# Performance work log

Hardware: AMD Instinct MI355X
Metric: run time of the kernel (lower is better)

The kernel has to match this reference:

```python
import jax, jax.numpy as jnp
import numpy as np

B, N, DIM = 2, 2048, 1024
H, DH = 16, 64
INNER = H * DH
SCALE = DH ** -0.5


def rotate_half(x):
    x1, x2 = jnp.split(x, 2, axis=-1)
    return jnp.concatenate((-x2, x1), axis=-1)


def apply_rotary(pos, t):
    # pos: [n, dh] broadcast against t: [b, h, n, dh]
    return t * jnp.cos(pos) + rotate_half(t) * jnp.sin(pos)


def setup_inputs() -> dict:
    key = jax.random.key(0)
    ks = jax.random.split(key, 5)
    x = jax.random.normal(ks[0], (B, N, DIM), dtype=jnp.float32)
    rotary_emb = jax.random.normal(ks[1], (N, DH), dtype=jnp.float32)
    w_qkv = jax.random.normal(ks[2], (3 * INNER, DIM), dtype=jnp.float32) * (DIM ** -0.5)
    w_out = jax.random.normal(ks[3], (DIM, INNER), dtype=jnp.float32) * (INNER ** -0.5)
    b_out = jax.random.normal(ks[4], (DIM,), dtype=jnp.float32) * 0.01
    return {"x": x, "rotary_emb": rotary_emb, "w_qkv": w_qkv, "w_out": w_out, "b_out": b_out}


def reference(x, rotary_emb, w_qkv, w_out, b_out):
    b, n, _ = x.shape
    qkv = jnp.einsum('bnd,ed->bne', x, w_qkv)  # [b, n, 3*inner]
    q, k, v = jnp.split(qkv, 3, axis=-1)
    # [b, n, inner] -> [b, h, n, dh]
    reshape = lambda t: t.reshape(b, n, H, DH).transpose(0, 2, 1, 3)
    q, k, v = reshape(q), reshape(k), reshape(v)
    q = apply_rotary(rotary_emb, q)
    k = apply_rotary(rotary_emb, k)
    dots = jnp.einsum('bhid,bhjd->bhij', q, k) * SCALE
    attn = jax.nn.softmax(dots, axis=-1)
    out = jnp.einsum('bhij,bhjd->bhid', attn, v)
    out = out.transpose(0, 2, 1, 3).reshape(b, n, INNER)
    return jnp.einsum('bne,de->bnd', out, w_out) + b_out
```

## Files before the change

kernel.cpp:

```cpp
#include <hip/hip_runtime.h>
#include <math.h>

typedef unsigned short ushort_t;
typedef __attribute__((ext_vector_type(8))) short short8v;
typedef __attribute__((ext_vector_type(4))) float float4v;

#define BB 2
#define NN 2048
#define HH 16
#define DHH 64
#define DIMM 1024
#define QKV3 3072
#define INNERR 1024
#define QSCALE 0.1803368801111244f

__device__ __forceinline__ ushort_t f2bf(float f) {
    unsigned u = __float_as_uint(f);
    u += 0x7fffu + ((u >> 16) & 1u);
    return (ushort_t)(u >> 16);
}
__device__ __forceinline__ float bf2f(unsigned h) {
    return __uint_as_float(h << 16);
}
__device__ __forceinline__ unsigned pk_bf16(float a, float b) {
#if __has_builtin(__builtin_amdgcn_cvt_pk_bf16_f32)
    typedef __attribute__((ext_vector_type(2))) __bf16 bf16x2;
    bf16x2 r = __builtin_amdgcn_cvt_pk_bf16_f32(a, b);
    return __builtin_bit_cast(unsigned, r);
#else
    return (unsigned)f2bf(a) | ((unsigned)f2bf(b) << 16);
#endif
}
__device__ __forceinline__ float fast_exp2(float x) {
#if __has_builtin(__builtin_amdgcn_exp2f)
    return __builtin_amdgcn_exp2f(x);
#else
    return exp2f(x);
#endif
}
__device__ __forceinline__ void gl2lds16(const void* g, void* l) {
    __builtin_amdgcn_global_load_lds(
        (const __attribute__((address_space(1))) unsigned int*)g,
        (__attribute__((address_space(3))) unsigned int*)l, 16, 0, 0);
}

__global__ __launch_bounds__(256) void conv_fused(const float* __restrict__ x,
                                                  const float* __restrict__ wqkv,
                                                  const float* __restrict__ wout,
                                                  ushort_t* __restrict__ xo,
                                                  ushort_t* __restrict__ wqkvo,
                                                  ushort_t* __restrict__ wouto) {
    int blk = blockIdx.x;
    const float* in; ushort_t* out; int i;
    if (blk < 4096)      { in = x;    out = xo;    i = blk * 256 + threadIdx.x; }
    else if (blk < 7168) { in = wqkv; out = wqkvo; i = (blk - 4096) * 256 + threadIdx.x; }
    else                 { in = wout; out = wouto; i = (blk - 7168) * 256 + threadIdx.x; }
    float4 v = ((const float4*)in)[i];
    ushort4 o;
    o.x = f2bf(v.x); o.y = f2bf(v.y); o.z = f2bf(v.z); o.w = f2bf(v.w);
    ((ushort4*)out)[i] = o;
}

template <int NOUT, bool BF16OUT, bool BIAS, bool ROT>
__global__ __launch_bounds__(256, 3) void gemm128(const ushort_t* __restrict__ A,
                                                  const ushort_t* __restrict__ Bm,
                                                  const float* __restrict__ bias,
                                                  const float* __restrict__ rot,
                                                  ushort_t* __restrict__ Vt,
                                                  void* __restrict__ Cout, int K) {
    constexpr int NCH = 4;
    __shared__ ushort_t As[2][128 * 32];
    __shared__ ushort_t Bs[2][128 * 32];
    const int t = threadIdx.x;
    const int lane = t & 63;
    const int w = t >> 6;
    const int wr = w >> 1;
    const int wc = w & 1;
    const int quad = lane >> 4;
    const int l15 = lane & 15;
    const int m0 = blockIdx.y * 128;
    const int n0 = blockIdx.x * 128;

    float4v acc[4][4];
#pragma unroll
    for (int i = 0; i < 4; ++i)
#pragma unroll
        for (int j = 0; j < 4; ++j) acc[i][j] = (float4v)0.0f;

    int srow[NCH], slc[NCH], sdst[NCH];
    bool sisA[NCH];
#pragma unroll
    for (int u = 0; u < NCH; ++u) {
        int c = u * 256 + t;
        if (c < 512) {
            int row = c >> 2;
            sisA[u] = true; srow[u] = row; slc[u] = (c & 3) ^ ((row >> 1) & 3); sdst[u] = c * 8;
        } else {
            int cb = c - 512;
            int row = cb >> 2;
            sisA[u] = false; srow[u] = row; slc[u] = (cb & 3) ^ ((row >> 1) & 3); sdst[u] = cb * 8;
        }
    }
#pragma unroll
    for (int u = 0; u < NCH; ++u) {
        if (sisA[u]) gl2lds16(&A[(size_t)(m0 + srow[u]) * K + slc[u] * 8], &As[0][sdst[u]]);
        else         gl2lds16(&Bm[(size_t)(n0 + srow[u]) * K + slc[u] * 8], &Bs[0][sdst[u]]);
    }
    const int NIT = K >> 5;
    for (int it = 0; it < NIT; ++it) {
        const int cur = it & 1;
        if (it + 1 < NIT) {
            const int nxt = cur ^ 1;
            const int kc = (it + 1) << 5;
#pragma unroll
            for (int u = 0; u < NCH; ++u) {
                if (sisA[u]) gl2lds16(&A[(size_t)(m0 + srow[u]) * K + kc + slc[u] * 8], &As[nxt][sdst[u]]);
                else         gl2lds16(&Bm[(size_t)(n0 + srow[u]) * K + kc + slc[u] * 8], &Bs[nxt][sdst[u]]);
            }
            asm volatile("s_waitcnt vmcnt(4)\n\ts_barrier" ::: "memory");
        } else {
            asm volatile("s_waitcnt vmcnt(0)\n\ts_barrier" ::: "memory");
        }
        short8v a[4], b[4];
#pragma unroll
        for (int i = 0; i < 4; ++i) {
            int row = wr * 64 + i * 16 + l15;
            int pc = quad ^ ((row >> 1) & 3);
            a[i] = *(const short8v*)&As[cur][row * 32 + pc * 8];
        }
#pragma unroll
        for (int j = 0; j < 4; ++j) {
            int row = wc * 64 + j * 16 + l15;
            int pc = quad ^ ((row >> 1) & 3);
            b[j] = *(const short8v*)&Bs[cur][row * 32 + pc * 8];
        }
#pragma unroll
        for (int i = 0; i < 4; ++i)
#pragma unroll
            for (int j = 0; j < 4; ++j)
                acc[i][j] = __builtin_amdgcn_mfma_f32_16x16x32_bf16(a[i], b[j], acc[i][j], 0, 0, 0);
        asm volatile("s_barrier" ::: "memory");
    }
    const int region = ROT ? (n0 >> 10) : 0;
    if (ROT && region == 2) {
#pragma unroll
        for (int i = 0; i < 4; ++i) {
            int grow = m0 + wr * 64 + i * 16 + quad * 4;
            int bb = grow >> 11, nn_ = grow & (NN - 1);
            int tk = nn_ & 63;
            int tp = (tk & 32) | ((tk & 12) << 1) | ((tk & 16) >> 2);
            int nstore = (nn_ & ~63) | tp;
#pragma unroll
            for (int j = 0; j < 4; ++j) {
                int vcol = n0 + wc * 64 + j * 16 + l15 - 2048;
                int hh = vcol >> 6, dh = vcol & 63;
                uint2 st;
                st.x = pk_bf16(acc[i][j][0], acc[i][j][1]);
                st.y = pk_bf16(acc[i][j][2], acc[i][j][3]);
                *(uint2*)&Vt[((size_t)(bb * HH + hh) * DHH + dh) * NN + nstore] = st;
            }
        }
        return;
    }
    if (ROT) {
        float scale = (region == 0) ? QSCALE : 1.0f;
#pragma unroll
        for (int i = 0; i < 4; ++i) {
#pragma unroll
            for (int r = 0; r < 4; ++r) {
                int n = (m0 + wr * 64 + i * 16 + quad * 4 + r) & (NN - 1);
#pragma unroll
                for (int jl = 0; jl < 2; ++jl) {
                    int dh = jl * 16 + l15;
                    float plo = rot[n * DHH + dh];
                    float phi = rot[n * DHH + dh + 32];
                    float lo = acc[i][jl][r], hi = acc[i][jl + 2][r];
                    acc[i][jl][r]     = (lo * __cosf(plo) - hi * __sinf(plo)) * scale;
                    acc[i][jl + 2][r] = (hi * __cosf(phi) + lo * __sinf(phi)) * scale;
                }
            }
        }
    }
#pragma unroll
    for (int i = 0; i < 4; ++i) {
        int grow = m0 + wr * 64 + i * 16 + quad * 4;
#pragma unroll
        for (int j = 0; j < 4; ++j) {
            int gcol = n0 + wc * 64 + j * 16 + l15;
            float bv = BIAS ? bias[gcol] : 0.0f;
#pragma unroll
            for (int r = 0; r < 4; ++r) {
                float v = acc[i][j][r] + bv;
                if (BF16OUT)
                    ((ushort_t*)Cout)[(size_t)(grow + r) * NOUT + gcol] = f2bf(v);
                else
                    ((float*)Cout)[(size_t)(grow + r) * NOUT + gcol] = v;
            }
        }
    }
}

template <int NOUT, bool BF16OUT, bool BIAS, bool ROT>
__global__ __launch_bounds__(256, 6) void gemm_bf16(const ushort_t* __restrict__ A,
                                                    const ushort_t* __restrict__ Bm,
                                                    const float* __restrict__ bias,
                                                    const float* __restrict__ rot,
                                                    ushort_t* __restrict__ Vt,
                                                    void* __restrict__ Cout, int K) {
    constexpr int NCH = 3;
    __shared__ ushort_t As[2][128 * 32];
    __shared__ ushort_t Bs[2][64 * 32];
    const int t = threadIdx.x;
    const int lane = t & 63;
    const int w = t >> 6;
    const int quad = lane >> 4;
    const int l15 = lane & 15;
    const int m0 = blockIdx.y * 128;
    const int n0 = blockIdx.x * 64;
    const int wm = w * 32;

    float4v acc[2][4];
#pragma unroll
    for (int i = 0; i < 2; ++i)
#pragma unroll
        for (int j = 0; j < 4; ++j) acc[i][j] = (float4v)0.0f;

    int srow[NCH], slc[NCH], sdst[NCH];
    bool sisA[NCH];
#pragma unroll
    for (int u = 0; u < NCH; ++u) {
        int c = u * 256 + t;
        if (c < 512) {
            int row = c >> 2;
            sisA[u] = true; srow[u] = row; slc[u] = (c & 3) ^ ((row >> 1) & 3); sdst[u] = c * 8;
        } else {
            int cb = c - 512;
            int row = cb >> 2;
            sisA[u] = false; srow[u] = row; slc[u] = (cb & 3) ^ ((row >> 1) & 3); sdst[u] = cb * 8;
        }
    }
#pragma unroll
    for (int u = 0; u < NCH; ++u) {
        if (sisA[u]) gl2lds16(&A[(size_t)(m0 + srow[u]) * K + slc[u] * 8], &As[0][sdst[u]]);
        else         gl2lds16(&Bm[(size_t)(n0 + srow[u]) * K + slc[u] * 8], &Bs[0][sdst[u]]);
    }
    const int NIT = K >> 5;
    for (int it = 0; it < NIT; ++it) {
        const int cur = it & 1;
        if (it + 1 < NIT) {
            const int nxt = cur ^ 1;
            const int kc = (it + 1) << 5;
#pragma unroll
            for (int u = 0; u < NCH; ++u) {
                if (sisA[u]) gl2lds16(&A[(size_t)(m0 + srow[u]) * K + kc + slc[u] * 8], &As[nxt][sdst[u]]);
                else         gl2lds16(&Bm[(size_t)(n0 + srow[u]) * K + kc + slc[u] * 8], &Bs[nxt][sdst[u]]);
            }
            asm volatile("s_waitcnt vmcnt(3)\n\ts_barrier" ::: "memory");
        } else {
            asm volatile("s_waitcnt vmcnt(0)\n\ts_barrier" ::: "memory");
        }
        short8v a[2], b[4];
#pragma unroll
        for (int i = 0; i < 2; ++i) {
            int row = wm + i * 16 + l15;
            int pc = quad ^ ((row >> 1) & 3);
            a[i] = *(const short8v*)&As[cur][row * 32 + pc * 8];
        }
#pragma unroll
        for (int j = 0; j < 4; ++j) {
            int row = j * 16 + l15;
            int pc = quad ^ ((row >> 1) & 3);
            b[j] = *(const short8v*)&Bs[cur][row * 32 + pc * 8];
        }
#pragma unroll
        for (int i = 0; i < 2; ++i)
#pragma unroll
            for (int j = 0; j < 4; ++j)
                acc[i][j] = __builtin_amdgcn_mfma_f32_16x16x32_bf16(a[i], b[j], acc[i][j], 0, 0, 0);
        asm volatile("s_barrier" ::: "memory");
    }
#pragma unroll
    for (int i = 0; i < 2; ++i) {
        int grow = m0 + wm + i * 16 + quad * 4;
#pragma unroll
        for (int j = 0; j < 4; ++j) {
            int gcol = n0 + j * 16 + l15;
            float bv = BIAS ? bias[gcol] : 0.0f;
#pragma unroll
            for (int r = 0; r < 4; ++r) {
                float v = acc[i][j][r] + bv;
                if (BF16OUT)
                    ((ushort_t*)Cout)[(size_t)(grow + r) * NOUT + gcol] = f2bf(v);
                else
                    ((float*)Cout)[(size_t)(grow + r) * NOUT + gcol] = v;
            }
        }
    }
}

__global__ __launch_bounds__(256, 2) void flash_mfma(const ushort_t* __restrict__ qkv,
                                                     const ushort_t* __restrict__ Vt,
                                                     ushort_t* __restrict__ po,
                                                     float* __restrict__ lp) {
    __shared__ ushort_t smem[16384];
    const int t = threadIdx.x;
    const int lane = t & 63;
    const int w = t >> 6;
    const int quad = lane >> 4;
    const int l15 = lane & 15;
    const int blk = blockIdx.x;
    const int slot = blk >> 3;
    const int ks = slot & 1;
    const int qt = (slot >> 1) & 7;
    const int bh = (blk & 7) * 4 + (slot >> 4);
    const int b = bh >> 4, h = bh & 15;
    const int n0 = qt * 256;

    short8v bq[4][2];
#pragma unroll
    for (int g = 0; g < 4; ++g) {
        size_t qb = (size_t)(b * NN + n0 + w * 64 + g * 16 + l15) * QKV3 + h * DHH + quad * 8;
        bq[g][0] = *(const short8v*)&qkv[qb];
        bq[g][1] = *(const short8v*)&qkv[qb + 32];
    }
    float4v o_acc[4][4];
    float4v l_acc[4];
#pragma unroll
    for (int g = 0; g < 4; ++g) {
        l_acc[g] = (float4v)0.0f;
#pragma unroll
        for (int nb = 0; nb < 4; ++nb) o_acc[g][nb] = (float4v)0.0f;
    }
    const short one_bf = (short)0x3F80;
    short8v ones8 = {one_bf, one_bf, one_bf, one_bf, one_bf, one_bf, one_bf, one_bf};
    const float4v ZR = (float4v)0.0f;

    const int s0 = t, s1 = 256 + t;
    const int r0 = s0 >> 3, lc0 = (s0 & 7) ^ (r0 & 7);
    const int r1 = s1 >> 3, lc1 = (s1 & 7) ^ (r1 & 7);
    const int koff0 = r0 * QKV3 + lc0 * 8, koff1 = r1 * QKV3 + lc1 * 8;
    const int voff0 = r0 * NN + lc0 * 8,   voff1 = r1 * NN + lc1 * 8;
    const ushort_t* kp = qkv + (size_t)b * NN * QKV3 + INNERR + h * DHH + (size_t)ks * 1024 * QKV3;
    const ushort_t* vp = Vt + (size_t)(b * HH + h) * DHH * NN + ks * 1024;

    {
        gl2lds16(kp + koff0, smem + 0 * 4096 + s0 * 8);
        gl2lds16(kp + koff1, smem + 0 * 4096 + s1 * 8);
        gl2lds16(vp + voff0, smem + 2 * 4096 + s0 * 8);
        gl2lds16(vp + voff1, smem + 2 * 4096 + s1 * 8);
    }
    for (int jt = 0; jt < 16; ++jt) {
        const int cur = jt & 1;
        if (jt < 15) {
            kp += 64 * QKV3;
            vp += 64;
            const int nxt = cur ^ 1;
            gl2lds16(kp + koff0, smem + nxt * 4096 + s0 * 8);
            gl2lds16(kp + koff1, smem + nxt * 4096 + s1 * 8);
            gl2lds16(vp + voff0, smem + (2 + nxt) * 4096 + s0 * 8);
            gl2lds16(vp + voff1, smem + (2 + nxt) * 4096 + s1 * 8);
            asm volatile("s_waitcnt vmcnt(4)\n\ts_barrier" ::: "memory");
        } else {
            asm volatile("s_waitcnt vmcnt(0)\n\ts_barrier" ::: "memory");
        }
        const ushort_t* Ksc = smem + cur * 4096;
        const ushort_t* Vtc = smem + (2 + cur) * 4096;
        short8v ak[2][4], bv[2][4];
#pragma unroll
        for (int nb = 0; nb < 4; ++nb) {
            int row = nb * 16 + l15;
            int base = row * 64;
            int r7 = row & 7;
            ak[0][nb] = *(const short8v*)&Ksc[base + ((quad) ^ r7) * 8];
            ak[1][nb] = *(const short8v*)&Ksc[base + ((4 + quad) ^ r7) * 8];
            bv[0][nb] = *(const short8v*)&Vtc[base + ((quad) ^ r7) * 8];
            bv[1][nb] = *(const short8v*)&Vtc[base + ((4 + quad) ^ r7) * 8];
        }
#pragma unroll
        for (int g = 0; g < 4; ++g) {
            float4v s[4];
#pragma unroll
            for (int nb = 0; nb < 4; ++nb)
                s[nb] = __builtin_amdgcn_mfma_f32_16x16x32_bf16(ak[0][nb], bq[g][0], ZR, 0, 0, 0);
#pragma unroll
            for (int nb = 0; nb < 4; ++nb)
                s[nb] = __builtin_amdgcn_mfma_f32_16x16x32_bf16(ak[1][nb], bq[g][1], s[nb], 0, 0, 0);
            float p[4][4];
#pragma unroll
            for (int nb = 0; nb < 4; ++nb)
#pragma unroll
                for (int r = 0; r < 4; ++r) p[nb][r] = fast_exp2(s[nb][r]);
            uint4 u0, u1;
            u0.x = pk_bf16(p[0][0], p[0][1]); u0.y = pk_bf16(p[0][2], p[0][3]);
            u0.z = pk_bf16(p[1][0], p[1][1]); u0.w = pk_bf16(p[1][2], p[1][3]);
            u1.x = pk_bf16(p[2][0], p[2][1]); u1.y = pk_bf16(p[2][2], p[2][3]);
            u1.z = pk_bf16(p[3][0], p[3][1]); u1.w = pk_bf16(p[3][2], p[3][3]);
            short8v ap0 = __builtin_bit_cast(short8v, u0);
            short8v ap1 = __builtin_bit_cast(short8v, u1);
            l_acc[g] = __builtin_amdgcn_mfma_f32_16x16x32_bf16(ap0, ones8, l_acc[g], 0, 0, 0);
            l_acc[g] = __builtin_amdgcn_mfma_f32_16x16x32_bf16(ap1, ones8, l_acc[g], 0, 0, 0);
#pragma unroll
            for (int nb = 0; nb < 4; ++nb) {
                o_acc[g][nb] = __builtin_amdgcn_mfma_f32_16x16x32_bf16(ap0, bv[0][nb], o_acc[g][nb], 0, 0, 0);
                o_acc[g][nb] = __builtin_amdgcn_mfma_f32_16x16x32_bf16(ap1, bv[1][nb], o_acc[g][nb], 0, 0, 0);
            }
        }
        asm volatile("s_barrier" ::: "memory");
    }
#pragma unroll
    for (int g = 0; g < 4; ++g) {
        if (l15 == 0)
            *(float4*)&lp[(size_t)(ks * 32 + bh) * NN + n0 + w * 64 + g * 16 + quad * 4] =
                *(float4*)&l_acc[g];
    }
    ushort_t* osc = smem + w * (32 * 68);
#pragma unroll
    for (int pass = 0; pass < 2; ++pass) {
#pragma unroll
        for (int gg = 0; gg < 2; ++gg) {
            int g = pass * 2 + gg;
#pragma unroll
            for (int nb = 0; nb < 4; ++nb)
#pragma unroll
                for (int r = 0; r < 4; ++r)
                    osc[(gg * 16 + quad * 4 + r) * 68 + nb * 16 + l15] = f2bf(o_acc[g][nb][r]);
        }
        __builtin_amdgcn_s_waitcnt(0);
        {
            int rr = lane >> 1, c0 = (lane & 1) * 32;
            size_t prow = ((size_t)(ks * 32 + bh) * NN + n0 + w * 64 + pass * 32 + rr) * DHH + c0;
#pragma unroll
            for (int u = 0; u < 4; ++u) {
                uint4 v = *(const uint4*)&osc[rr * 68 + c0 + u * 8];
                *(uint4*)&po[prow + u * 8] = v;
            }
        }
        __builtin_amdgcn_s_waitcnt(0);
    }
}

__global__ __launch_bounds__(256) void reduce_o(const ushort_t* __restrict__ po,
                                                const float* __restrict__ lp,
                                                ushort_t* __restrict__ attn) {
    int tg = blockIdx.x * 256 + threadIdx.x;
    int bh = tg >> 15;
    int rem = tg & 32767;
    int n = rem >> 4;
    int dh0 = (rem & 15) * 4;
    size_t p0 = ((size_t)bh * NN + n) * DHH + dh0;
    size_t p1 = p0 + (size_t)32 * NN * DHH;
    uint2 a = *(const uint2*)&po[p0];
    uint2 c = *(const uint2*)&po[p1];
    float inv = 1.0f / (lp[(size_t)bh * NN + n] + lp[(size_t)(32 + bh) * NN + n]);
    float o0 = (bf2f(a.x & 0xffff) + bf2f(c.x & 0xffff)) * inv;
    float o1 = (bf2f(a.x >> 16)    + bf2f(c.x >> 16))    * inv;
    float o2 = (bf2f(a.y & 0xffff) + bf2f(c.y & 0xffff)) * inv;
    float o3 = (bf2f(a.y >> 16)    + bf2f(c.y >> 16))    * inv;
    int b = bh >> 4, h = bh & 15;
    uint2 st;
    st.x = pk_bf16(o0, o1);
    st.y = pk_bf16(o2, o3);
    *(uint2*)&attn[((size_t)(b * NN + n)) * INNERR + h * DHH + dh0] = st;
}

extern "C" void kernel_launch(void* const* d_in, const int* in_sizes, int n_in,
                              void* d_out, int out_size, void* d_ws, size_t ws_size,
                              hipStream_t stream) {
    const float* x = (const float*)d_in[0];
    const float* rot = (const float*)d_in[1];
    const float* w_qkv = (const float*)d_in[2];
    const float* w_out = (const float*)d_in[3];
    const float* b_out = (const float*)d_in[4];
    float* y = (float*)d_out;

    char* ws = (char*)d_ws;
    ushort_t* qkv_bf  = (ushort_t*)(ws);
    ushort_t* vt_bf   = (ushort_t*)(ws + 25165824);
    ushort_t* wout_bf = (ushort_t*)(ws + 33554432);
    ushort_t* wqkv_bf = (ushort_t*)(ws + 35651584);
    float*    lp      = (float*)(ws + 35651584);
    ushort_t* x_bf    = (ushort_t*)(ws + 41943040);
    ushort_t* attn_bf = x_bf;
    ushort_t* po      = (ushort_t*)(ws + 50331648);

    conv_fused<<<8192, 256, 0, stream>>>(x, w_qkv, w_out, x_bf, wqkv_bf, wout_bf);
    gemm128<QKV3, true, false, true><<<dim3(24, 32), 256, 0, stream>>>(
        x_bf, wqkv_bf, nullptr, rot, vt_bf, qkv_bf, DIMM);
    flash_mfma<<<512, 256, 0, stream>>>(qkv_bf, vt_bf, po, lp);
    reduce_o<<<4096, 256, 0, stream>>>(po, lp, attn_bf);
    gemm_bf16<INNERR, false, true, false><<<dim3(16, 32), 256, 0, stream>>>(
        attn_bf, wout_bf, b_out, nullptr, nullptr, y, INNERR);
}
```

Measured before the change: 188.8 us.

## Double KV tile per barrier to 128 keys and raise wave priority around MFMA

The flash attention loop now stages 128 keys per iteration (two 64-key halves) in double-buffered LDS, which doubles shared memory to 64KB and halves the number of barrier/wait iterations. It also wraps the MFMA compute section in s_setprio so compute waves are favoured over loads. The aim is to cut synchronization overhead and overlap more memory with compute. The cost is higher LDS use, which may limit occupancy at two blocks per CU.

```diff
diff --git a/kernel.cpp b/kernel.cpp
--- a/kernel.cpp
+++ b/kernel.cpp
@@ -302,7 +302,7 @@
                                                      const ushort_t* __restrict__ Vt,
                                                      ushort_t* __restrict__ po,
                                                      float* __restrict__ lp) {
-    __shared__ ushort_t smem[16384];
+    __shared__ ushort_t smem[32768];
     const int t = threadIdx.x;
     const int lane = t & 63;
     const int w = t >> 6;
@@ -335,75 +335,87 @@
     short8v ones8 = {one_bf, one_bf, one_bf, one_bf, one_bf, one_bf, one_bf, one_bf};
     const float4v ZR = (float4v)0.0f;
 
-    const int s0 = t, s1 = 256 + t;
-    const int r0 = s0 >> 3, lc0 = (s0 & 7) ^ (r0 & 7);
-    const int r1 = s1 >> 3, lc1 = (s1 & 7) ^ (r1 & 7);
-    const int koff0 = r0 * QKV3 + lc0 * 8, koff1 = r1 * QKV3 + lc1 * 8;
-    const int voff0 = r0 * NN + lc0 * 8,   voff1 = r1 * NN + lc1 * 8;
+    int kgo[4], vgo[4], ldst[4];
+#pragma unroll
+    for (int u = 0; u < 4; ++u) {
+        int c = u * 256 + t;
+        int half = c >> 9;
+        int cl = c & 511;
+        int row = cl >> 3;
+        int lc = (c & 7) ^ (row & 7);
+        kgo[u] = (half * 64 + row) * QKV3 + lc * 8;
+        vgo[u] = row * NN + half * 64 + lc * 8;
+        ldst[u] = half * 4096 + cl * 8;
+    }
     const ushort_t* kp = qkv + (size_t)b * NN * QKV3 + INNERR + h * DHH + (size_t)ks * 1024 * QKV3;
     const ushort_t* vp = Vt + (size_t)(b * HH + h) * DHH * NN + ks * 1024;
 
-    {
-        gl2lds16(kp + koff0, smem + 0 * 4096 + s0 * 8);
-        gl2lds16(kp + koff1, smem + 0 * 4096 + s1 * 8);
-        gl2lds16(vp + voff0, smem + 2 * 4096 + s0 * 8);
-        gl2lds16(vp + voff1, smem + 2 * 4096 + s1 * 8);
-    }
-    for (int jt = 0; jt < 16; ++jt) {
+#pragma unroll
+    for (int u = 0; u < 4; ++u) {
+        gl2lds16(kp + kgo[u], smem + ldst[u]);
+        gl2lds16(vp + vgo[u], smem + 8192 + ldst[u]);
+    }
+    for (int jt = 0; jt < 8; ++jt) {
         const int cur = jt & 1;
-        if (jt < 15) {
-            kp += 64 * QKV3;
-            vp += 64;
-            const int nxt = cur ^ 1;
-            gl2lds16(kp + koff0, smem + nxt * 4096 + s0 * 8);
-            gl2lds16(kp + koff1, smem + nxt * 4096 + s1 * 8);
-            gl2lds16(vp + voff0, smem + (2 + nxt) * 4096 + s0 * 8);
-            gl2lds16(vp + voff1, smem + (2 + nxt) * 4096 + s1 * 8);
-            asm volatile("s_waitcnt vmcnt(4)\n\ts_barrier" ::: "memory");
+        if (jt < 7) {
+            kp += 128 * QKV3;
+            vp += 128;
+            const int nb_ = (cur ^ 1) * 16384;
+#pragma unroll
+            for (int u = 0; u < 4; ++u) {
+                gl2lds16(kp + kgo[u], smem + nb_ + ldst[u]);
+                gl2lds16(vp + vgo[u], smem + nb_ + 8192 + ldst[u]);
+            }
+            asm volatile("s_waitcnt vmcnt(8)\n\ts_barrier" ::: "memory");
         } else {
             asm volatile("s_waitcnt vmcnt(0)\n\ts_barrier" ::: "memory");
         }
-        const ushort_t* Ksc = smem + cur * 4096;
-        const ushort_t* Vtc = smem + (2 + cur) * 4096;
-        short8v ak[2][4], bv[2][4];
-#pragma unroll
-        for (int nb = 0; nb < 4; ++nb) {
-            int row = nb * 16 + l15;
-            int base = row * 64;
-            int r7 = row & 7;
-            ak[0][nb] = *(const short8v*)&Ksc[base + ((quad) ^ r7) * 8];
-            ak[1][nb] = *(const short8v*)&Ksc[base + ((4 + quad) ^ r7) * 8];
-            bv[0][nb] = *(const short8v*)&Vtc[base + ((quad) ^ r7) * 8];
-            bv[1][nb] = *(const short8v*)&Vtc[base + ((4 + quad) ^ r7) * 8];
-        }
-#pragma unroll
-        for (int g = 0; g < 4; ++g) {
-            float4v s[4];
-#pragma unroll
-            for (int nb = 0; nb < 4; ++nb)
-                s[nb] = __builtin_amdgcn_mfma_f32_16x16x32_bf16(ak[0][nb], bq[g][0], ZR, 0, 0, 0);
-#pragma unroll
-            for (int nb = 0; nb < 4; ++nb)
-                s[nb] = __builtin_amdgcn_mfma_f32_16x16x32_bf16(ak[1][nb], bq[g][1], s[nb], 0, 0, 0);
-            float p[4][4];
-#pragma unroll
-            for (int nb = 0; nb < 4; ++nb)
-#pragma unroll
-                for (int r = 0; r < 4; ++r) p[nb][r] = fast_exp2(s[nb][r]);
-            uint4 u0, u1;
-            u0.x = pk_bf16(p[0][0], p[0][1]); u0.y = pk_bf16(p[0][2], p[0][3]);
-            u0.z = pk_bf16(p[1][0], p[1][1]); u0.w = pk_bf16(p[1][2], p[1][3]);
-            u1.x = pk_bf16(p[2][0], p[2][1]); u1.y = pk_bf16(p[2][2], p[2][3]);
-            u1.z = pk_bf16(p[3][0], p[3][1]); u1.w = pk_bf16(p[3][2], p[3][3]);
-            short8v ap0 = __builtin_bit_cast(short8v, u0);
-            short8v ap1 = __builtin_bit_cast(short8v, u1);
-            l_acc[g] = __builtin_amdgcn_mfma_f32_16x16x32_bf16(ap0, ones8, l_acc[g], 0, 0, 0);
-            l_acc[g] = __builtin_amdgcn_mfma_f32_16x16x32_bf16(ap1, ones8, l_acc[g], 0, 0, 0);
+#pragma unroll
+        for (int hf = 0; hf < 2; ++hf) {
+            const ushort_t* Ksc = smem + cur * 16384 + hf * 4096;
+            const ushort_t* Vtc = smem + cur * 16384 + 8192 + hf * 4096;
+            short8v ak[2][4], bv[2][4];
 #pragma unroll
             for (int nb = 0; nb < 4; ++nb) {
-                o_acc[g][nb] = __builtin_amdgcn_mfma_f32_16x16x32_bf16(ap0, bv[0][nb], o_acc[g][nb], 0, 0, 0);
-                o_acc[g][nb] = __builtin_amdgcn_mfma_f32_16x16x32_bf16(ap1, bv[1][nb], o_acc[g][nb], 0, 0, 0);
-            }
+                int row = nb * 16 + l15;
+                int base = row * 64;
+                int r7 = row & 7;
+                ak[0][nb] = *(const short8v*)&Ksc[base + ((quad) ^ r7) * 8];
+                ak[1][nb] = *(const short8v*)&Ksc[base + ((4 + quad) ^ r7) * 8];
+                bv[0][nb] = *(const short8v*)&Vtc[base + ((quad) ^ r7) * 8];
+                bv[1][nb] = *(const short8v*)&Vtc[base + ((4 + quad) ^ r7) * 8];
+            }
+            __builtin_amdgcn_s_setprio(1);
+#pragma unroll
+            for (int g = 0; g < 4; ++g) {
+                float4v s[4];
+#pragma unroll
+                for (int nb = 0; nb < 4; ++nb)
+                    s[nb] = __builtin_amdgcn_mfma_f32_16x16x32_bf16(ak[0][nb], bq[g][0], ZR, 0, 0, 0);
+#pragma unroll
+                for (int nb = 0; nb < 4; ++nb)
+                    s[nb] = __builtin_amdgcn_mfma_f32_16x16x32_bf16(ak[1][nb], bq[g][1], s[nb], 0, 0, 0);
+                float p[4][4];
+#pragma unroll
+                for (int nb = 0; nb < 4; ++nb)
+#pragma unroll
+                    for (int r = 0; r < 4; ++r) p[nb][r] = fast_exp2(s[nb][r]);
+                uint4 u0, u1;
+                u0.x = pk_bf16(p[0][0], p[0][1]); u0.y = pk_bf16(p[0][2], p[0][3]);
+                u0.z = pk_bf16(p[1][0], p[1][1]); u0.w = pk_bf16(p[1][2], p[1][3]);
+                u1.x = pk_bf16(p[2][0], p[2][1]); u1.y = pk_bf16(p[2][2], p[2][3]);
+                u1.z = pk_bf16(p[3][0], p[3][1]); u1.w = pk_bf16(p[3][2], p[3][3]);
+                short8v ap0 = __builtin_bit_cast(short8v, u0);
+                short8v ap1 = __builtin_bit_cast(short8v, u1);
+                l_acc[g] = __builtin_amdgcn_mfma_f32_16x16x32_bf16(ap0, ones8, l_acc[g], 0, 0, 0);
+                l_acc[g] = __builtin_amdgcn_mfma_f32_16x16x32_bf16(ap1, ones8, l_acc[g], 0, 0, 0);
+#pragma unroll
+                for (int nb = 0; nb < 4; ++nb) {
+                    o_acc[g][nb] = __builtin_amdgcn_mfma_f32_16x16x32_bf16(ap0, bv[0][nb], o_acc[g][nb], 0, 0, 0);
+                    o_acc[g][nb] = __builtin_amdgcn_mfma_f32_16x16x32_bf16(ap1, bv[1][nb], o_acc[g][nb], 0, 0, 0);
+                }
+            }
+            __builtin_amdgcn_s_setprio(0);
         }
         asm volatile("s_barrier" ::: "memory");
     }
```

After: 190.5 us. Within noise of the previous version (+0.9%).

## Drop split-K flash attention, fuse normalization, remove reduce kernel

Applied to the files above, without the earlier changes.

Replaces the two-way key split (each block covering 256 queries over half the keys, followed by a separate reduce kernel) with blocks that cover 128 queries over all keys and normalize in the epilogue using a reciprocal of the row sum. This removes the partial-output and row-sum round trips through global memory and one kernel launch. In exchange each block runs twice as many key tiles while reusing each loaded K/V tile across fewer queries, which doubles total K/V traffic from LDS. It also raises wave priority with s_setprio around the MFMA section and computes both Q-group score tiles before the softmax to interleave work.

```diff
diff --git a/kernel.cpp b/kernel.cpp
--- a/kernel.cpp
+++ b/kernel.cpp
@@ -36,6 +36,13 @@
     return __builtin_amdgcn_exp2f(x);
 #else
     return exp2f(x);
+#endif
+}
+__device__ __forceinline__ float fast_rcp(float x) {
+#if __has_builtin(__builtin_amdgcn_rcpf)
+    return __builtin_amdgcn_rcpf(x);
+#else
+    return 1.0f / x;
 #endif
 }
 __device__ __forceinline__ void gl2lds16(const void* g, void* l) {
@@ -300,8 +307,7 @@
 
 __global__ __launch_bounds__(256, 2) void flash_mfma(const ushort_t* __restrict__ qkv,
                                                      const ushort_t* __restrict__ Vt,
-                                                     ushort_t* __restrict__ po,
-                                                     float* __restrict__ lp) {
+                                                     ushort_t* __restrict__ attn) {
     __shared__ ushort_t smem[16384];
     const int t = threadIdx.x;
     const int lane = t & 63;
@@ -310,23 +316,22 @@
     const int l15 = lane & 15;
     const int blk = blockIdx.x;
     const int slot = blk >> 3;
-    const int ks = slot & 1;
-    const int qt = (slot >> 1) & 7;
+    const int qt = slot & 15;
     const int bh = (blk & 7) * 4 + (slot >> 4);
     const int b = bh >> 4, h = bh & 15;
-    const int n0 = qt * 256;
-
-    short8v bq[4][2];
-#pragma unroll
-    for (int g = 0; g < 4; ++g) {
-        size_t qb = (size_t)(b * NN + n0 + w * 64 + g * 16 + l15) * QKV3 + h * DHH + quad * 8;
+    const int n0 = qt * 128;
+
+    short8v bq[2][2];
+#pragma unroll
+    for (int g = 0; g < 2; ++g) {
+        size_t qb = (size_t)(b * NN + n0 + w * 32 + g * 16 + l15) * QKV3 + h * DHH + quad * 8;
         bq[g][0] = *(const short8v*)&qkv[qb];
         bq[g][1] = *(const short8v*)&qkv[qb + 32];
     }
-    float4v o_acc[4][4];
-    float4v l_acc[4];
-#pragma unroll
-    for (int g = 0; g < 4; ++g) {
+    float4v o_acc[2][4];
+    float4v l_acc[2];
+#pragma unroll
+    for (int g = 0; g < 2; ++g) {
         l_acc[g] = (float4v)0.0f;
 #pragma unroll
         for (int nb = 0; nb < 4; ++nb) o_acc[g][nb] = (float4v)0.0f;
@@ -340,8 +345,8 @@
     const int r1 = s1 >> 3, lc1 = (s1 & 7) ^ (r1 & 7);
     const int koff0 = r0 * QKV3 + lc0 * 8, koff1 = r1 * QKV3 + lc1 * 8;
     const int voff0 = r0 * NN + lc0 * 8,   voff1 = r1 * NN + lc1 * 8;
-    const ushort_t* kp = qkv + (size_t)b * NN * QKV3 + INNERR + h * DHH + (size_t)ks * 1024 * QKV3;
-    const ushort_t* vp = Vt + (size_t)(b * HH + h) * DHH * NN + ks * 1024;
+    const ushort_t* kp = qkv + (size_t)b * NN * QKV3 + INNERR + h * DHH;
+    const ushort_t* vp = Vt + (size_t)(b * HH + h) * DHH * NN;
 
     {
         gl2lds16(kp + koff0, smem + 0 * 4096 + s0 * 8);
@@ -349,9 +354,9 @@
         gl2lds16(vp + voff0, smem + 2 * 4096 + s0 * 8);
         gl2lds16(vp + voff1, smem + 2 * 4096 + s1 * 8);
     }
-    for (int jt = 0; jt < 16; ++jt) {
+    for (int jt = 0; jt < 32; ++jt) {
         const int cur = jt & 1;
-        if (jt < 15) {
+        if (jt < 31) {
             kp += 64 * QKV3;
             vp += 64;
             const int nxt = cur ^ 1;
@@ -376,20 +381,28 @@
             bv[0][nb] = *(const short8v*)&Vtc[base + ((quad) ^ r7) * 8];
             bv[1][nb] = *(const short8v*)&Vtc[base + ((4 + quad) ^ r7) * 8];
         }
-#pragma unroll
-        for (int g = 0; g < 4; ++g) {
-            float4v s[4];
+        __builtin_amdgcn_s_setprio(1);
+        float4v s0v[4], s1v[4];
+#pragma unroll
+        for (int nb = 0; nb < 4; ++nb)
+            s0v[nb] = __builtin_amdgcn_mfma_f32_16x16x32_bf16(ak[0][nb], bq[0][0], ZR, 0, 0, 0);
+#pragma unroll
+        for (int nb = 0; nb < 4; ++nb)
+            s0v[nb] = __builtin_amdgcn_mfma_f32_16x16x32_bf16(ak[1][nb], bq[0][1], s0v[nb], 0, 0, 0);
+#pragma unroll
+        for (int nb = 0; nb < 4; ++nb)
+            s1v[nb] = __builtin_amdgcn_mfma_f32_16x16x32_bf16(ak[0][nb], bq[1][0], ZR, 0, 0, 0);
+#pragma unroll
+        for (int nb = 0; nb < 4; ++nb)
+            s1v[nb] = __builtin_amdgcn_mfma_f32_16x16x32_bf16(ak[1][nb], bq[1][1], s1v[nb], 0, 0, 0);
+#pragma unroll
+        for (int g = 0; g < 2; ++g) {
+            float4v* sv = (g == 0) ? s0v : s1v;
+            float p[4][4];
 #pragma unroll
             for (int nb = 0; nb < 4; ++nb)
-                s[nb] = __builtin_amdgcn_mfma_f32_16x16x32_bf16(ak[0][nb], bq[g][0], ZR, 0, 0, 0);
-#pragma unroll
-            for (int nb = 0; nb < 4; ++nb)
-                s[nb] = __builtin_amdgcn_mfma_f32_16x16x32_bf16(ak[1][nb], bq[g][1], s[nb], 0, 0, 0);
-            float p[4][4];
-#pragma unroll
-            for (int nb = 0; nb < 4; ++nb)
-#pragma unroll
-                for (int r = 0; r < 4; ++r) p[nb][r] = fast_exp2(s[nb][r]);
+#pragma unroll
+                for (int r = 0; r < 4; ++r) p[nb][r] = fast_exp2(sv[nb][r]);
             uint4 u0, u1;
             u0.x = pk_bf16(p[0][0], p[0][1]); u0.y = pk_bf16(p[0][2], p[0][3]);
             u0.z = pk_bf16(p[1][0], p[1][1]); u0.w = pk_bf16(p[1][2], p[1][3]);
@@ -405,62 +418,32 @@
                 o_acc[g][nb] = __builtin_amdgcn_mfma_f32_16x16x32_bf16(ap1, bv[1][nb], o_acc[g][nb], 0, 0, 0);
             }
         }
+        __builtin_amdgcn_s_setprio(0);
         asm volatile("s_barrier" ::: "memory");
     }
-#pragma unroll
-    for (int g = 0; g < 4; ++g) {
-        if (l15 == 0)
-            *(float4*)&lp[(size_t)(ks * 32 + bh) * NN + n0 + w * 64 + g * 16 + quad * 4] =
-                *(float4*)&l_acc[g];
-    }
+    float inv[2][4];
+#pragma unroll
+    for (int g = 0; g < 2; ++g)
+#pragma unroll
+        for (int r = 0; r < 4; ++r) inv[g][r] = fast_rcp(l_acc[g][r]);
     ushort_t* osc = smem + w * (32 * 68);
 #pragma unroll
-    for (int pass = 0; pass < 2; ++pass) {
-#pragma unroll
-        for (int gg = 0; gg < 2; ++gg) {
-            int g = pass * 2 + gg;
-#pragma unroll
-            for (int nb = 0; nb < 4; ++nb)
-#pragma unroll
-                for (int r = 0; r < 4; ++r)
-                    osc[(gg * 16 + quad * 4 + r) * 68 + nb * 16 + l15] = f2bf(o_acc[g][nb][r]);
-        }
-        __builtin_amdgcn_s_waitcnt(0);
-        {
-            int rr = lane >> 1, c0 = (lane & 1) * 32;
-            size_t prow = ((size_t)(ks * 32 + bh) * NN + n0 + w * 64 + pass * 32 + rr) * DHH + c0;
-#pragma unroll
-            for (int u = 0; u < 4; ++u) {
-                uint4 v = *(const uint4*)&osc[rr * 68 + c0 + u * 8];
-                *(uint4*)&po[prow + u * 8] = v;
-            }
-        }
-        __builtin_amdgcn_s_waitcnt(0);
-    }
-}
-
-__global__ __launch_bounds__(256) void reduce_o(const ushort_t* __restrict__ po,
-                                                const float* __restrict__ lp,
-                                                ushort_t* __restrict__ attn) {
-    int tg = blockIdx.x * 256 + threadIdx.x;
-    int bh = tg >> 15;
-    int rem = tg & 32767;
-    int n = rem >> 4;
-    int dh0 = (rem & 15) * 4;
-    size_t p0 = ((size_t)bh * NN + n) * DHH + dh0;
-    size_t p1 = p0 + (size_t)32 * NN * DHH;
-    uint2 a = *(const uint2*)&po[p0];
-    uint2 c = *(const uint2*)&po[p1];
-    float inv = 1.0f / (lp[(size_t)bh * NN + n] + lp[(size_t)(32 + bh) * NN + n]);
-    float o0 = (bf2f(a.x & 0xffff) + bf2f(c.x & 0xffff)) * inv;
-    float o1 = (bf2f(a.x >> 16)    + bf2f(c.x >> 16))    * inv;
-    float o2 = (bf2f(a.y & 0xffff) + bf2f(c.y & 0xffff)) * inv;
-    float o3 = (bf2f(a.y >> 16)    + bf2f(c.y >> 16))    * inv;
-    int b = bh >> 4, h = bh & 15;
-    uint2 st;
-    st.x = pk_bf16(o0, o1);
-    st.y = pk_bf16(o2, o3);
-    *(uint2*)&attn[((size_t)(b * NN + n)) * INNERR + h * DHH + dh0] = st;
+    for (int g = 0; g < 2; ++g)
+#pragma unroll
+        for (int nb = 0; nb < 4; ++nb)
+#pragma unroll
+            for (int r = 0; r < 4; ++r)
+                osc[(g * 16 + quad * 4 + r) * 68 + nb * 16 + l15] = f2bf(o_acc[g][nb][r] * inv[g][r]);
+    __builtin_amdgcn_s_waitcnt(0);
+    {
+        int rr = lane >> 1, c0 = (lane & 1) * 32;
+        size_t arow = ((size_t)(b * NN + n0 + w * 32 + rr)) * INNERR + h * DHH + c0;
+#pragma unroll
+        for (int u = 0; u < 4; ++u) {
+            uint4 v = *(const uint4*)&osc[rr * 68 + c0 + u * 8];
+            *(uint4*)&attn[arow + u * 8] = v;
+        }
+    }
 }
 
 extern "C" void kernel_launch(void* const* d_in, const int* in_sizes, int n_in,
@@ -478,16 +461,13 @@
     ushort_t* vt_bf   = (ushort_t*)(ws + 25165824);
     ushort_t* wout_bf = (ushort_t*)(ws + 33554432);
     ushort_t* wqkv_bf = (ushort_t*)(ws + 35651584);
-    float*    lp      = (float*)(ws + 35651584);
     ushort_t* x_bf    = (ushort_t*)(ws + 41943040);
     ushort_t* attn_bf = x_bf;
-    ushort_t* po      = (ushort_t*)(ws + 50331648);
 
     conv_fused<<<8192, 256, 0, stream>>>(x, w_qkv, w_out, x_bf, wqkv_bf, wout_bf);
     gemm128<QKV3, true, false, true><<<dim3(24, 32), 256, 0, stream>>>(
         x_bf, wqkv_bf, nullptr, rot, vt_bf, qkv_bf, DIMM);
-    flash_mfma<<<512, 256, 0, stream>>>(qkv_bf, vt_bf, po, lp);
-    reduce_o<<<4096, 256, 0, stream>>>(po, lp, attn_bf);
+    flash_mfma<<<512, 256, 0, stream>>>(qkv_bf, vt_bf, attn_bf);
     gemm_bf16<INNERR, false, true, false><<<dim3(16, 32), 256, 0, stream>>>(
         attn_bf, wout_bf, b_out, nullptr, nullptr, y, INNERR);
 }
```

Result: faster. 183.2 us (-3.0%).
